# Performance work log

Measured on AMD Instinct MI355X. Metric: run time of the kernel, lower is better.

## Reference

```python
import jax, jax.numpy as jnp
import numpy as np
from jax import lax

DILATION = 2
EPS = 1e-05


def _scales_and_weights(img_sz):
    m = min(img_sz)
    if m > 128:
        return [m // 16, m // 8, m // 4], [0.8, 0.1, 0.1]
    elif m > 64:
        return [m // 4, m // 2], [0.4, 0.6]
    else:
        return [m // 2], [1.0]


def _box_conv(z, ksz, stride):
    # all-ones 3D box filter, VALID padding, rhs (kernel) dilation = 2
    kern = jnp.ones((1, 1, ksz, ksz, ksz), dtype=z.dtype)
    return lax.conv_general_dilated(
        z, kern,
        window_strides=(stride, stride, stride),
        padding='VALID',
        rhs_dilation=(DILATION, DILATION, DILATION),
        dimension_numbers=('NCDHW', 'OIDHW', 'NCDHW'))


def setup_inputs() -> dict:
    key = jax.random.key(0)
    k1, k2 = jax.random.split(key)
    shape = (4, 1, 128, 128, 128)
    return {
        'input': jax.random.normal(k1, shape, dtype=jnp.float32),
        'target': jax.random.normal(k2, shape, dtype=jnp.float32),
    }


def reference(input, target):
    img_sz = input.shape[2:]
    scales, weights = _scales_and_weights(list(img_sz))
    B = input.shape[0]

    input_2 = input ** 2
    target_2 = target ** 2
    input_target = input * target

    lncc_total = jnp.asarray(0.0, dtype=input.dtype)
    for ksz, w in zip(scales, weights):
        step = max((ksz + 1) // 2, 1)
        conv = lambda z: _box_conv(z, ksz, step).reshape(B, -1)
        x_sum = conv(input)
        y_sum = conv(target)
        x2_sum = conv(input_2)
        y2_sum = conv(target_2)
        xy_sum = conv(input_target)

        numel = float(ksz ** 3)
        x_mean = x_sum / numel
        y_mean = y_sum / numel
        cross = xy_sum - y_mean * x_sum - x_mean * y_sum + y_mean * x_mean * numel
        x_var = x2_sum - 2 * x_mean * x_sum + x_mean ** 2 * numel
        y_var = y2_sum - 2 * y_mean * y_sum + y_mean ** 2 * numel
        lncc = cross * cross / (x_var * y_var + EPS)
        lncc_total = lncc_total + (1.0 - lncc.mean()) * w
    return lncc_total
```

## Files before the change

kernel.cpp:

```cpp
#include <hip/hip_runtime.h>


#define NSTAT 5

__global__ __launch_bounds__(256) void lncc_pass1(
    const float* __restrict__ x, const float* __restrict__ y,
    float* __restrict__ chunks ) {
  const int blk = blockIdx.x;
  const int b  = blk >> 6;
  const int ci = (blk >> 3) & 7;
  const int cj = blk & 7;
  const int tid = threadIdx.x;
  const int w4 = tid & 31;
  const int s  = tid >> 5;
  const size_t base = (size_t)b * (128u * 128u * 128u)
                    + (size_t)(16 * cj + 2 * s) * 128 + (size_t)w4 * 4;

  float sx = 0.f, sy = 0.f, sx2 = 0.f, sy2 = 0.f, sxy = 0.f;
#pragma unroll
  for (int i = 0; i < 8; ++i) {
    size_t off = base + (size_t)(16 * ci + 2 * i) * (128 * 128);
    float4 a = *(const float4*)(x + off);
    float4 t = *(const float4*)(y + off);
    sx  += a.x + a.z;
    sy  += t.x + t.z;
    sx2 += a.x * a.x + a.z * a.z;
    sy2 += t.x * t.x + t.z * t.z;
    sxy += a.x * t.x + a.z * t.z;
  }

  __shared__ float sd[256 * NSTAT];
  sd[tid]        = sx;
  sd[256 + tid]  = sy;
  sd[512 + tid]  = sx2;
  sd[768 + tid]  = sy2;
  sd[1024 + tid] = sxy;
  __syncthreads();

  if (tid < 40) {
    const int k = tid >> 3, ck = tid & 7;
    float acc = 0.f;
#pragma unroll
    for (int sdi = 0; sdi < 8; ++sdi)
#pragma unroll
      for (int j = 0; j < 4; ++j)
        acc += sd[k * 256 + sdi * 32 + ck * 4 + j];
    const int c = ci * 64 + cj * 8 + ck;
    chunks[((size_t)b * 512 + c) * NSTAT + k] = acc;
  }
}

__global__ __launch_bounds__(512) void lncc_pass2(
    const float* __restrict__ chunks, float* __restrict__ out) {
  const int tid = threadIdx.x;
  __shared__ float s5[2048 * NSTAT];
  for (int i = tid; i < 2048 * NSTAT; i += 512) s5[i] = chunks[i];
  __syncthreads();

  __shared__ double part[8 * NSTAT];
  __shared__ double totl[4 * NSTAT];
  for (int b = 0; b < 4; ++b) {
    double vv[NSTAT];
    const int cbase = (b * 512 + tid) * NSTAT;
#pragma unroll
    for (int k = 0; k < NSTAT; ++k) vv[k] = (double)s5[cbase + k];
#pragma unroll
    for (int off = 32; off; off >>= 1)
#pragma unroll
      for (int k = 0; k < NSTAT; ++k) vv[k] += __shfl_down(vv[k], off);
    if ((tid & 63) == 0)
#pragma unroll
      for (int k = 0; k < NSTAT; ++k) part[(tid >> 6) * NSTAT + k] = vv[k];
    __syncthreads();
    if (tid < NSTAT) {
      double sum = 0.0;
      for (int w = 0; w < 8; ++w) sum += part[w * NSTAT + tid];
      totl[b * NSTAT + tid] = sum;
    }
    __syncthreads();
  }

  double lncc = 0.0;
  if (tid < 500) {
    const int b = tid / 125, rem = tid % 125;
    const int od = rem / 25, oh = (rem / 5) % 5, ow = rem % 5;
    double a0 = 0, a1 = 0, a2 = 0, a3 = 0, a4 = 0;
    for (int ci = od; ci < od + 4; ++ci)
      for (int cj = oh; cj < oh + 4; ++cj)
        for (int ck = ow; ck < ow + 4; ++ck) {
          const int idx = (b * 512 + ci * 64 + cj * 8 + ck) * NSTAT;
          a0 += s5[idx];     a1 += s5[idx + 1];
          a2 += s5[idx + 2]; a3 += s5[idx + 3];
          a4 += s5[idx + 4];
        }
    const double numel = 32768.0;
    const double cross = a4 - a0 * a1 / numel;
    const double xvar  = a2 - a0 * a0 / numel;
    const double yvar  = a3 - a1 * a1 / numel;
    lncc = cross * cross / (xvar * yvar + 1e-5);
  }
#pragma unroll
  for (int off = 32; off; off >>= 1) lncc += __shfl_down(lncc, off);
  __shared__ double dred[8];
  if ((tid & 63) == 0) dred[tid >> 6] = lncc;
  __syncthreads();

  if (tid == 0) {
    double sum32 = 0.0;
    for (int i = 0; i < 8; ++i) sum32 += dred[i];
    const double mean32 = sum32 / 500.0;
    double sum64 = 0.0;
    for (int b = 0; b < 4; ++b) {
      const double X  = totl[b * NSTAT + 0], Y  = totl[b * NSTAT + 1];
      const double X2 = totl[b * NSTAT + 2], Y2 = totl[b * NSTAT + 3];
      const double XY = totl[b * NSTAT + 4];
      const double numel = 262144.0;
      const double cross = XY - X * Y / numel;
      const double xvar  = X2 - X * X / numel;
      const double yvar  = Y2 - Y * Y / numel;
      sum64 += cross * cross / (xvar * yvar + 1e-5);
    }
    const double mean64 = sum64 * 0.25;
    out[0] = (float)((1.0 - mean32) * 0.4 + (1.0 - mean64) * 0.6);
  }
}

extern "C" void kernel_launch(void* const* d_in, const int* in_sizes, int n_in,
                              void* d_out, int out_size, void* d_ws, size_t ws_size,
                              hipStream_t stream) {
  const float* x = (const float*)d_in[0];
  const float* y = (const float*)d_in[1];
  float* chunks = (float*)d_ws;
  lncc_pass1<<<256, 256, 0, stream>>>(x, y, chunks);
  lncc_pass2<<<1, 512, 0, stream>>>(chunks, (float*)d_out);
}
```

Before: 103.4 us.

## Fuse two-pass LNCC reduction into one kernel with last-block atomic finish

```diff
diff --git a/kernel.cpp b/kernel.cpp
--- a/kernel.cpp
+++ b/kernel.cpp
@@ -3,9 +3,9 @@
 
 #define NSTAT 5
 
-__global__ __launch_bounds__(256) void lncc_pass1(
+__global__ __launch_bounds__(256) void lncc_fused(
     const float* __restrict__ x, const float* __restrict__ y,
-    float* __restrict__ chunks ) {
+    float* ws , unsigned* counter, float* out) {
   const int blk = blockIdx.x;
   const int b  = blk >> 6;
   const int ci = (blk >> 3) & 7;
@@ -14,12 +14,12 @@
   const int w4 = tid & 31;
   const int s  = tid >> 5;
   const size_t base = (size_t)b * (128u * 128u * 128u)
-                    + (size_t)(16 * cj + 2 * s) * 128 + (size_t)w4 * 4;
+                    + (size_t)(16 * cj + 2 * s) * 128 + (size_t)(w4 * 4);
 
   float sx = 0.f, sy = 0.f, sx2 = 0.f, sy2 = 0.f, sxy = 0.f;
 #pragma unroll
   for (int i = 0; i < 8; ++i) {
-    size_t off = base + (size_t)(16 * ci + 2 * i) * (128 * 128);
+    size_t off = base + (size_t)((16 * ci + 2 * i) * (128 * 128));
     float4 a = *(const float4*)(x + off);
     float4 t = *(const float4*)(y + off);
     sx  += a.x + a.z;
@@ -45,83 +45,80 @@
 #pragma unroll
       for (int j = 0; j < 4; ++j)
         acc += sd[k * 256 + sdi * 32 + ck * 4 + j];
-    const int c = ci * 64 + cj * 8 + ck;
-    chunks[((size_t)b * 512 + c) * NSTAT + k] = acc;
+    ws[((b * 512) + ci * 64 + cj * 8 + ck) * NSTAT + k] = acc;
   }
-}
 
-__global__ __launch_bounds__(512) void lncc_pass2(
-    const float* __restrict__ chunks, float* __restrict__ out) {
-  const int tid = threadIdx.x;
+  __threadfence();
+  __syncthreads();
+  __shared__ unsigned lastflag;
+  if (tid == 0) lastflag = (atomicAdd(counter, 1u) == 255u) ? 1u : 0u;
+  __syncthreads();
+  if (!lastflag) return;
+  __threadfence();
+
   __shared__ float s5[2048 * NSTAT];
-  for (int i = tid; i < 2048 * NSTAT; i += 512) s5[i] = chunks[i];
+  for (int i = tid; i < 2048 * NSTAT / 4; i += 256)
+    ((float4*)s5)[i] = ((const float4*)ws)[i];
   __syncthreads();
 
-  __shared__ double part[8 * NSTAT];
-  __shared__ double totl[4 * NSTAT];
-  for (int b = 0; b < 4; ++b) {
-    double vv[NSTAT];
-    const int cbase = (b * 512 + tid) * NSTAT;
+  const int wave = tid >> 6, lane = tid & 63;
+
+  float tot[NSTAT] = {0.f, 0.f, 0.f, 0.f, 0.f};
+  for (int c = lane; c < 512; c += 64) {
+    const int idx = (wave * 512 + c) * NSTAT;
 #pragma unroll
-    for (int k = 0; k < NSTAT; ++k) vv[k] = (double)s5[cbase + k];
+    for (int k = 0; k < NSTAT; ++k) tot[k] += s5[idx + k];
+  }
 #pragma unroll
-    for (int off = 32; off; off >>= 1)
+  for (int off = 32; off; off >>= 1)
 #pragma unroll
-      for (int k = 0; k < NSTAT; ++k) vv[k] += __shfl_down(vv[k], off);
-    if ((tid & 63) == 0)
+    for (int k = 0; k < NSTAT; ++k) tot[k] += __shfl_down(tot[k], off);
+  __shared__ float totl[4 * NSTAT];
+  if (lane == 0)
 #pragma unroll
-      for (int k = 0; k < NSTAT; ++k) part[(tid >> 6) * NSTAT + k] = vv[k];
-    __syncthreads();
-    if (tid < NSTAT) {
-      double sum = 0.0;
-      for (int w = 0; w < 8; ++w) sum += part[w * NSTAT + tid];
-      totl[b * NSTAT + tid] = sum;
-    }
-    __syncthreads();
-  }
+    for (int k = 0; k < NSTAT; ++k) totl[wave * NSTAT + k] = tot[k];
+  __syncthreads();
 
-  double lncc = 0.0;
-  if (tid < 500) {
-    const int b = tid / 125, rem = tid % 125;
+  float lsum = 0.f;
+  for (int wd = tid; wd < 500; wd += 256) {
+    const int b2 = wd / 125, rem = wd % 125;
     const int od = rem / 25, oh = (rem / 5) % 5, ow = rem % 5;
-    double a0 = 0, a1 = 0, a2 = 0, a3 = 0, a4 = 0;
-    for (int ci = od; ci < od + 4; ++ci)
-      for (int cj = oh; cj < oh + 4; ++cj)
-        for (int ck = ow; ck < ow + 4; ++ck) {
-          const int idx = (b * 512 + ci * 64 + cj * 8 + ck) * NSTAT;
+    float a0 = 0.f, a1 = 0.f, a2 = 0.f, a3 = 0.f, a4 = 0.f;
+    for (int i = od; i < od + 4; ++i)
+      for (int j = oh; j < oh + 4; ++j)
+        for (int k2 = ow; k2 < ow + 4; ++k2) {
+          const int idx = ((b2 * 512) + i * 64 + j * 8 + k2) * NSTAT;
           a0 += s5[idx];     a1 += s5[idx + 1];
           a2 += s5[idx + 2]; a3 += s5[idx + 3];
           a4 += s5[idx + 4];
         }
-    const double numel = 32768.0;
-    const double cross = a4 - a0 * a1 / numel;
-    const double xvar  = a2 - a0 * a0 / numel;
-    const double yvar  = a3 - a1 * a1 / numel;
-    lncc = cross * cross / (xvar * yvar + 1e-5);
+    const float numel = 32768.f;
+    const float cross = a4 - a0 * a1 / numel;
+    const float xv    = a2 - a0 * a0 / numel;
+    const float yv    = a3 - a1 * a1 / numel;
+    lsum += cross * cross / (xv * yv + 1e-5f);
   }
 #pragma unroll
-  for (int off = 32; off; off >>= 1) lncc += __shfl_down(lncc, off);
-  __shared__ double dred[8];
-  if ((tid & 63) == 0) dred[tid >> 6] = lncc;
+  for (int off = 32; off; off >>= 1) lsum += __shfl_down(lsum, off);
+  __shared__ float wred[4];
+  if (lane == 0) wred[wave] = lsum;
   __syncthreads();
 
   if (tid == 0) {
-    double sum32 = 0.0;
-    for (int i = 0; i < 8; ++i) sum32 += dred[i];
-    const double mean32 = sum32 / 500.0;
-    double sum64 = 0.0;
-    for (int b = 0; b < 4; ++b) {
-      const double X  = totl[b * NSTAT + 0], Y  = totl[b * NSTAT + 1];
-      const double X2 = totl[b * NSTAT + 2], Y2 = totl[b * NSTAT + 3];
-      const double XY = totl[b * NSTAT + 4];
-      const double numel = 262144.0;
-      const double cross = XY - X * Y / numel;
-      const double xvar  = X2 - X * X / numel;
-      const double yvar  = Y2 - Y * Y / numel;
-      sum64 += cross * cross / (xvar * yvar + 1e-5);
+    const float mean32 = (wred[0] + wred[1] + wred[2] + wred[3]) / 500.f;
+    float sum64 = 0.f;
+    for (int bb = 0; bb < 4; ++bb) {
+      const float X  = totl[bb * NSTAT + 0], Y  = totl[bb * NSTAT + 1];
+      const float X2 = totl[bb * NSTAT + 2], Y2 = totl[bb * NSTAT + 3];
+      const float XY = totl[bb * NSTAT + 4];
+      const float numel = 262144.f;
+      const float cross = XY - X * Y / numel;
+      const float xv    = X2 - X * X / numel;
+      const float yv    = Y2 - Y * Y / numel;
+      sum64 += cross * cross / (xv * yv + 1e-5f);
     }
-    const double mean64 = sum64 * 0.25;
-    out[0] = (float)((1.0 - mean32) * 0.4 + (1.0 - mean64) * 0.6);
+    const float mean64 = sum64 * 0.25f;
+    out[0] = (1.f - mean32) * 0.4f + (1.f - mean64) * 0.6f;
   }
 }
 
@@ -130,7 +127,8 @@
                               hipStream_t stream) {
   const float* x = (const float*)d_in[0];
   const float* y = (const float*)d_in[1];
-  float* chunks = (float*)d_ws;
-  lncc_pass1<<<256, 256, 0, stream>>>(x, y, chunks);
-  lncc_pass2<<<1, 512, 0, stream>>>(chunks, (float*)d_out);
+  float* ws = (float*)d_ws;
+  unsigned* counter = (unsigned*)((char*)d_ws + 40960);
+  hipMemsetAsync(counter, 0, sizeof(unsigned), stream);
+  lncc_fused<<<256, 256, 0, stream>>>(x, y, ws, counter, (float*)d_out);
 }
```

New measurement: 124.2 us. 1.2x slower.
